# Performance work log

Hardware: AMD Instinct MI355X
Metric: run time of the kernel (lower is better)

## Reference

```python
import jax, jax.numpy as jnp
import numpy as np

STRIDES = (8, 16, 32)
INPUT = (640, 640)
NC = 80           # num_classes
CONF = 0.65       # conf_thr
IOU_THR = 0.65    # nms iou_threshold
K = 1000          # fixed candidate cap for jit-compatible NMS (padded/masked)


def _priors():
    # MlvlPointGenerator(offset=0, with_stride=True): per level, points at
    # (x*stride, y*stride) flattened y-major, format [cx, cy, stride, stride].
    ps = []
    for s in STRIDES:
        H, W = INPUT[0] // s, INPUT[1] // s
        yy, xx = jnp.meshgrid(jnp.arange(H, dtype=jnp.float32),
                              jnp.arange(W, dtype=jnp.float32), indexing='ij')
        cx = (xx * s).ravel()
        cy = (yy * s).ravel()
        st = jnp.full_like(cx, float(s))
        ps.append(jnp.stack([cx, cy, st, st], axis=-1))
    return jnp.concatenate(ps, axis=0)  # [8400, 4]


def _flatten(xs, c):
    # permute(0,2,3,1).reshape(B, -1, c) per level, concat over priors
    return jnp.concatenate(
        [x.transpose(0, 2, 3, 1).reshape(x.shape[0], -1, c) for x in xs], axis=1)


def _decode(priors, bp):
    # bp: [B, N, 4]; priors: [N, 4] (cx, cy, sw, sh)
    xys = bp[..., :2] * priors[:, 2:] + priors[:, :2]
    whs = jnp.exp(bp[..., 2:]) * priors[:, 2:]
    tl = xys - whs * 0.5
    br = xys + whs * 0.5
    return jnp.concatenate([tl, br], axis=-1)  # [B, N, 4] tlbr


def _iou(a, b):
    tl = jnp.maximum(a[:, None, :2], b[None, :, :2])
    br = jnp.minimum(a[:, None, 2:], b[None, :, 2:])
    wh = jnp.clip(br - tl, 0.0)
    inter = wh[..., 0] * wh[..., 1]
    area = lambda x: (x[:, 2] - x[:, 0]) * (x[:, 3] - x[:, 1])
    union = area(a)[:, None] + area(b)[None, :] - inter
    return inter / (union + 1e-6)


def _nms_single(cls_s, obj_s, boxes):
    # cls_s: [N, NC] sigmoid scores; obj_s: [N]; boxes: [N, 4]
    max_s = cls_s.max(axis=-1)
    labels = jnp.argmax(cls_s, axis=-1)
    score = max_s * obj_s
    valid = score >= CONF                       # confidence mask
    sc = jnp.where(valid, score, 0.0)
    top_sc, idx = jax.lax.top_k(sc, K)          # sorted descending -> greedy order
    b = boxes[idx]
    lab = labels[idx]
    v = valid[idx]
    # class-aware (batched) NMS: offset boxes per label so classes never overlap
    max_coord = jnp.max(jnp.abs(b)) + 1.0
    ob = b + (lab.astype(b.dtype) * max_coord)[:, None]
    iou = _iou(ob, ob)                          # [K, K]
    j = jnp.arange(K)
    def body(i, keep):
        sup = (iou[i] > IOU_THR) & (j > i)
        return jnp.where(keep[i] & v[i], keep & (~sup), keep)
    keep = jax.lax.fori_loop(0, K, body, jnp.ones(K, dtype=bool))
    final = keep & v
    dets = jnp.where(final[:, None],
                     jnp.concatenate([b, top_sc[:, None]], axis=-1), 0.0)  # [K, 5]
    labs = jnp.where(final, lab, -1)
    return dets, labs, final


def setup_inputs() -> dict:
    key = jax.random.key(0)
    ks = jax.random.split(key, 9)
    B = 32
    shapes = {
        'cls0': (B, NC, 80, 80), 'cls1': (B, NC, 40, 40), 'cls2': (B, NC, 20, 20),
        'bbox0': (B, 4, 80, 80), 'bbox1': (B, 4, 40, 40), 'bbox2': (B, 4, 20, 20),
        'obj0': (B, 1, 80, 80), 'obj1': (B, 1, 40, 40), 'obj2': (B, 1, 20, 20),
    }
    return {n: jax.random.normal(k, s, dtype=jnp.float32)
            for (n, s), k in zip(shapes.items(), ks)}


def reference(cls0, cls1, cls2, bbox0, bbox1, bbox2, obj0, obj1, obj2):
    priors = _priors()
    cls = jax.nn.sigmoid(_flatten([cls0, cls1, cls2], NC))       # [B, 8400, 80]
    bp = _flatten([bbox0, bbox1, bbox2], 4)                      # [B, 8400, 4]
    obj = jax.nn.sigmoid(_flatten([obj0, obj1, obj2], 1)[..., 0])  # [B, 8400]
    boxes = _decode(priors, bp)                                  # [B, 8400, 4]
    # per-image class-wise batched NMS, padded to K detections
    dets, labels, keep = jax.vmap(_nms_single)(cls, obj, boxes)
    return dets, labels, keep
```

## Files before the change

### kernel.cpp

```cpp
#include <hip/hip_runtime.h>
#include <stdint.h>

#define NPRIOR 8400
#define NB 32
#define NCLS 80
#define KTOP 1000
#define CAP 8400
#define CPAD 16
#define PCH 8
#define CPC 10

typedef unsigned long long u64;

__device__ __forceinline__ float exp_np(float x) {
#pragma clang fp contract(off)
    if (x > 88.72283935546875f) return __builtin_huge_valf();
    if (x < -87.3365478515625f) return 0.0f;
    float q = rintf(x * 1.442695040f);
    float r = fmaf(q, -6.93145752e-1f, x);
    r = fmaf(q, -1.42860677e-6f, r);
    float p = fmaf(1.9875691500e-4f, r, 1.3981999507e-3f);
    p = fmaf(p, r, 8.3334519073e-3f);
    p = fmaf(p, r, 4.1665795894e-2f);
    p = fmaf(p, r, 1.6666665459e-1f);
    p = fmaf(p, r, 5.0000001201e-1f);
    float r2 = r * r;
    p = fmaf(p, r2, r);
    p = p + 1.0f;
    return ldexpf(p, (int)q);
}
__device__ __forceinline__ float sigm_np(float x) {
#pragma clang fp contract(off)
    float t = exp_np(-x);
    return 1.0f / (1.0f + t);
}

__device__ __forceinline__ void level_of(int n, int& W, int& s, int& loc) {
    if (n < 6400)      { W = 80; s = 8;  loc = n; }
    else if (n < 8000) { W = 40; s = 16; loc = n - 6400; }
    else               { W = 20; s = 32; loc = n - 8000; }
}

__device__ float4 decode32(int b, int n,
                           const float* bb0, const float* bb1, const float* bb2) {
#pragma clang fp contract(off)
    int W, s, loc; level_of(n, W, s, loc);
    const float* bb = (s == 8) ? bb0 : (s == 16) ? bb1 : bb2;
    int hw = W * W;
    int y = loc / W, x = loc - y * W;
    const float* bp = bb + (size_t)b * 4 * hw + y * W + x;
    float fs = (float)s;
    float cx = (float)x * fs, cy = (float)y * fs;
    float xc = bp[0] * fs + cx;
    float yc = bp[hw] * fs + cy;
    float wv = exp_np(bp[2 * hw]) * fs;
    float hv = exp_np(bp[3 * hw]) * fs;
    float wv2 = wv * 0.5f, hv2 = hv * 0.5f;
    float4 r;
    r.x = xc - wv2;
    r.y = yc - hv2;
    r.z = xc + wv2;
    r.w = yc + hv2;
    return r;
}

__device__ __forceinline__ u64 packkc(float s, int c) {
    return ((u64)__float_as_uint(s) << 32) | (unsigned)(~(unsigned)c);
}

__global__ void __launch_bounds__(256) score1_k(
    const float* __restrict__ cls0, const float* __restrict__ cls1, const float* __restrict__ cls2,
    u64* __restrict__ part)
{
#pragma clang fp contract(off)
    int b = blockIdx.z, ch = blockIdx.y;
    int g = blockIdx.x * 256 + threadIdx.x;
    if (g >= NPRIOR / 4) return;
    int n0 = g * 4;
    int W, s, loc; level_of(n0, W, s, loc);
    const float* cls = (s == 8) ? cls0 : (s == 16) ? cls1 : cls2;
    int hw = W * W;
    int y = loc / W, x = loc - y * W;
    const float* cp = cls + (size_t)b * NCLS * hw + y * W + x;

    int c0 = ch * CPC;
    float4 v = *(const float4*)(cp + (size_t)c0 * hw);
    u64 k0 = packkc(sigm_np(v.x), c0);
    u64 k1 = packkc(sigm_np(v.y), c0);
    u64 k2 = packkc(sigm_np(v.z), c0);
    u64 k3 = packkc(sigm_np(v.w), c0);
#pragma unroll
    for (int cc = 1; cc < CPC; ++cc) {
        int c = c0 + cc;
        v = *(const float4*)(cp + (size_t)c * hw);
        u64 t;
        t = packkc(sigm_np(v.x), c); if (t > k0) k0 = t;
        t = packkc(sigm_np(v.y), c); if (t > k1) k1 = t;
        t = packkc(sigm_np(v.z), c); if (t > k2) k2 = t;
        t = packkc(sigm_np(v.w), c); if (t > k3) k3 = t;
    }
    u64* p = part + ((size_t)ch * NB + b) * NPRIOR + n0;
    p[0] = k0; p[1] = k1; p[2] = k2; p[3] = k3;
}

__global__ void __launch_bounds__(256) score2_k(
    const float* __restrict__ ob0, const float* __restrict__ ob1, const float* __restrict__ ob2,
    const u64* __restrict__ part,
    float* __restrict__ sc, int* __restrict__ labels,
    u64* __restrict__ keys, int* __restrict__ cnts)
{
#pragma clang fp contract(off)
    int b = blockIdx.y;
    int g = blockIdx.x * 256 + threadIdx.x;
    if (g >= NPRIOR / 4) return;
    int n0 = g * 4;
    int W, s, loc; level_of(n0, W, s, loc);
    const float* ob = (s == 8) ? ob0 : (s == 16) ? ob1 : ob2;
    int hw = W * W;
    int y = loc / W, x = loc - y * W;

    u64 k0 = 0, k1 = 0, k2 = 0, k3 = 0;
#pragma unroll
    for (int ch = 0; ch < PCH; ++ch) {
        const u64* p = part + ((size_t)ch * NB + b) * NPRIOR + n0;
        u64 t0 = p[0], t1 = p[1], t2 = p[2], t3 = p[3];
        if (t0 > k0) k0 = t0;
        if (t1 > k1) k1 = t1;
        if (t2 > k2) k2 = t2;
        if (t3 > k3) k3 = t3;
    }
    float4 tM;
    tM.x = __uint_as_float((unsigned)(k0 >> 32));
    tM.y = __uint_as_float((unsigned)(k1 >> 32));
    tM.z = __uint_as_float((unsigned)(k2 >> 32));
    tM.w = __uint_as_float((unsigned)(k3 >> 32));
    int4 lab;
    lab.x = (int)(~(unsigned)(k0 & 0xffffffffull));
    lab.y = (int)(~(unsigned)(k1 & 0xffffffffull));
    lab.z = (int)(~(unsigned)(k2 & 0xffffffffull));
    lab.w = (int)(~(unsigned)(k3 & 0xffffffffull));

    float4 o = *(const float4*)(ob + (size_t)b * hw + y * W + x);
    float4 sv;
    sv.x = tM.x * sigm_np(o.x);
    sv.y = tM.y * sigm_np(o.y);
    sv.z = tM.z * sigm_np(o.z);
    sv.w = tM.w * sigm_np(o.w);
    float4 scv;
    scv.x = (sv.x >= 0.65f) ? sv.x : 0.0f;
    scv.y = (sv.y >= 0.65f) ? sv.y : 0.0f;
    scv.z = (sv.z >= 0.65f) ? sv.z : 0.0f;
    scv.w = (sv.w >= 0.65f) ? sv.w : 0.0f;
    *(float4*)(sc + (size_t)b * NPRIOR + n0) = scv;
    *(int4*)(labels + (size_t)b * NPRIOR + n0) = lab;

    int lane = threadIdx.x & 63;
#pragma unroll
    for (int e = 0; e < 4; ++e) {
        float se = (e == 0) ? scv.x : (e == 1) ? scv.y : (e == 2) ? scv.z : scv.w;
        bool val = se > 0.0f;
        u64 mb = __ballot(val);
        if (mb) {
            int lead = (int)__builtin_ctzll(mb);
            int base = 0;
            if (lane == lead) base = atomicAdd(&cnts[b * CPAD], (int)__popcll(mb));
            base = __shfl(base, lead);
            if (val) {
                int myoff = (int)__popcll(mb & ((1ull << lane) - 1ull));
                keys[(size_t)b * CAP + base + myoff] =
                    ((u64)__float_as_uint(se) << 32) | (unsigned)(~(unsigned)(n0 + e));
            }
        }
    }
}

__global__ void __launch_bounds__(256) rank_part(
    const u64* __restrict__ keys, const int* __restrict__ cnts,
    int* __restrict__ rankbuf)
{
    int b = blockIdx.y, tid = threadIdx.x;
    int cn = min(cnts[b * CPAD], CAP);
    int nt = (cn + 255) >> 8;
    int ntt = nt * nt;
    const u64* keyimg = keys + (size_t)b * CAP;
    int lane = tid & 63;

    for (int t = blockIdx.x; t < ntt; t += gridDim.x) {
        int it = t / nt, jt = t - it * nt;
        int i = it * 256 + tid;
        u64 ki = (i < cn) ? keyimg[i] : ~0ull;
        int rank = 0;
        int jbase = jt * 256;
        int jend = min(jbase + 256, cn);
        for (int jb = jbase; jb < jend; jb += 64) {
            int j = jb + lane;
            u64 kv = (j < cn) ? keyimg[j] : 0ull;
            unsigned lo = (unsigned)kv, hi = (unsigned)(kv >> 32);
            int lim = jend - jb;
#pragma unroll
            for (int l = 0; l < 64; ++l) {
                unsigned jlo = __builtin_amdgcn_readlane(lo, l);
                unsigned jhi = __builtin_amdgcn_readlane(hi, l);
                u64 kj = ((u64)jhi << 32) | jlo;
                rank += (l < lim && kj > ki) ? 1 : 0;
            }
        }
        if (i < cn && rank > 0) atomicAdd(&rankbuf[(size_t)b * CAP + i], rank);
    }
}

__global__ void __launch_bounds__(256) scatter_k(
    const u64* __restrict__ keys, const int* __restrict__ cnts,
    const int* __restrict__ rankbuf,
    const float* __restrict__ sc, const int* __restrict__ labels,
    const float* __restrict__ bb0, const float* __restrict__ bb1, const float* __restrict__ bb2,
    float4* __restrict__ sel_box, float* __restrict__ sel_score,
    int* __restrict__ sel_label, int* __restrict__ maxbits, u64* __restrict__ vmask)
{
#pragma clang fp contract(off)
    __shared__ float redbuf[256];
    int b = blockIdx.y, chunk = blockIdx.x, tid = threadIdx.x;
    int cn = min(cnts[b * CPAD], CAP);
    int base = chunk * 256;
    if (chunk != 0 && base >= cn) return;

    const u64* keyimg = keys + (size_t)b * CAP;
    const int* labb = labels + (size_t)b * NPRIOR;
    const float* scb = sc + (size_t)b * NPRIOR;

    int i = base + tid;
    float lmax = 0.0f;
    if (i < cn) {
        int rank = rankbuf[(size_t)b * CAP + i];
        if (rank < KTOP) {
            u64 ki = keyimg[i];
            unsigned n = ~(unsigned)(ki & 0xffffffffull);
            float s = __uint_as_float((unsigned)(ki >> 32));
            float4 bx = decode32(b, (int)n, bb0, bb1, bb2);
            sel_box[(size_t)b * 1024 + rank] = bx;
            sel_score[(size_t)b * 1024 + rank] = s;
            sel_label[(size_t)b * 1024 + rank] = labb[n];
            lmax = fmaxf(fmaxf(fabsf(bx.x), fabsf(bx.y)),
                         fmaxf(fabsf(bx.z), fabsf(bx.w)));
        }
    }

    if (chunk == 0) {
        if (cn < KTOP && tid == 0) {
            float lm = 0.0f;
            int r = cn;
            for (int n = 0; n < NPRIOR && r < KTOP; ++n) {
                if (scb[n] == 0.0f) {
                    float4 bx = decode32(b, n, bb0, bb1, bb2);
                    sel_box[(size_t)b * 1024 + r] = bx;
                    sel_score[(size_t)b * 1024 + r] = 0.0f;
                    sel_label[(size_t)b * 1024 + r] = labb[n];
                    lm = fmaxf(lm, fmaxf(fmaxf(fabsf(bx.x), fabsf(bx.y)),
                                         fmaxf(fabsf(bx.z), fabsf(bx.w))));
                    ++r;
                }
            }
            lmax = fmaxf(lmax, lm);
        }
        if (tid < 24) {
            sel_box[(size_t)b * 1024 + 1000 + tid] = make_float4(0.f, 0.f, 0.f, 0.f);
            sel_score[(size_t)b * 1024 + 1000 + tid] = 0.0f;
            sel_label[(size_t)b * 1024 + 1000 + tid] = 0;
        }
        if (tid < 16) {
            int vc = min(cn, KTOP);
            int lo = tid * 64;
            u64 m;
            if (vc >= lo + 64)      m = ~0ull;
            else if (vc <= lo)      m = 0ull;
            else                    m = (1ull << (vc - lo)) - 1ull;
            vmask[b * 16 + tid] = m;
        }
    }

    redbuf[tid] = lmax;
    __syncthreads();
    for (int off = 128; off > 0; off >>= 1) {
        if (tid < off) redbuf[tid] = fmaxf(redbuf[tid], redbuf[tid + off]);
        __syncthreads();
    }
    if (tid == 0) atomicMax(&maxbits[b * CPAD], __float_as_int(redbuf[0]));
}

__global__ void __launch_bounds__(256) build_mask_T(
    const float4* __restrict__ sel_box, const int* __restrict__ sel_label,
    const int* __restrict__ maxbits, u64* __restrict__ Cmask)
{
#pragma clang fp contract(off)
    __shared__ float4 obr[256];
    __shared__ float arr[256];
    int b = blockIdx.y;
    int cg = blockIdx.x & 15, rgq = blockIdx.x >> 4;
    if (rgq * 4 > cg) return;
    int tid = threadIdx.x, wave = tid >> 6, lane = tid & 63;
    float mc = __int_as_float(maxbits[b * CPAD]) + 1.0f;

    {
        int row = rgq * 256 + tid;
        float4 v = sel_box[(size_t)b * 1024 + row];
        float off = (float)sel_label[(size_t)b * 1024 + row] * mc;
        v.x += off; v.y += off; v.z += off; v.w += off;
        obr[tid] = v;
        arr[tid] = (v.z - v.x) * (v.w - v.y);
    }
    int col = cg * 64 + lane;
    float4 a = sel_box[(size_t)b * 1024 + col];
    float offc = (float)sel_label[(size_t)b * 1024 + col] * mc;
    a.x += offc; a.y += offc; a.z += offc; a.w += offc;
    float ac = (a.z - a.x) * (a.w - a.y);
    __syncthreads();

    int rg = rgq * 4 + wave;
    if (rg > cg) return;
    int rowbase = rg * 64;
    u64 bits = 0;
#pragma unroll 8
    for (int r = 0; r < 64; ++r) {
        int row = rowbase + r;
        float4 rb = obr[wave * 64 + r];
        float ra = arr[wave * 64 + r];
        bool pred = false;
        if (row < col && row < KTOP && col < KTOP) {
            float tlx = fmaxf(rb.x, a.x), tly = fmaxf(rb.y, a.y);
            float brx = fminf(rb.z, a.z), bry = fminf(rb.w, a.w);
            float w = fmaxf(brx - tlx, 0.0f), h = fmaxf(bry - tly, 0.0f);
            float inter = w * h;
            float uni = (ra + ac) - inter;
            float iou = inter / (uni + 1e-6f);
            pred = iou > 0.65f;
        }
        bits |= pred ? (1ull << r) : 0ull;
    }
    Cmask[((size_t)b * 16 + rg) * 1024 + col] = bits;
}

__global__ void __launch_bounds__(64) nms_fixpoint_write(
    const u64* __restrict__ Cmask, const u64* __restrict__ vmask,
    const float4* __restrict__ sel_box, const float* __restrict__ sel_score,
    const int* __restrict__ sel_label, float* __restrict__ out)
{
    int b = blockIdx.x, lane = threadIdx.x;
    const u64* Cimg = Cmask + (size_t)b * 16 * 1024;
    u64 Khist[16];
#pragma unroll
    for (int g = 0; g < 16; ++g) {
        int col = g * 64 + lane;
        bool supp = false;
#pragma unroll
        for (int gp = 0; gp < g; ++gp)
            supp |= (Cimg[(size_t)gp * 1024 + col] & Khist[gp]) != 0ull;
        u64 V = vmask[b * 16 + g] & ~__ballot(supp);
        u64 T = Cimg[(size_t)g * 1024 + col];
        u64 K = V;
        for (int it = 0; it < 64; ++it) {
            u64 Knew = V & ~__ballot((T & K) != 0ull);
            if (Knew == K) break;
            K = Knew;
        }
        Khist[g] = K;
    }

    const size_t selo = (size_t)b * 1024;
    float* lab_o = out + (size_t)NB * KTOP * 5;
    float* keep_o = lab_o + (size_t)NB * KTOP;
#pragma unroll
    for (int g = 0; g < 16; ++g) {
        int k = g * 64 + lane;
        if (k >= KTOP) break;
        bool fin = (Khist[g] >> lane) & 1ull;
        float4 bx = sel_box[selo + k];
        float s = sel_score[selo + k];
        int lb = sel_label[selo + k];
        size_t o5 = ((size_t)b * KTOP + k) * 5;
        out[o5 + 0] = fin ? bx.x : 0.0f;
        out[o5 + 1] = fin ? bx.y : 0.0f;
        out[o5 + 2] = fin ? bx.z : 0.0f;
        out[o5 + 3] = fin ? bx.w : 0.0f;
        out[o5 + 4] = fin ? s : 0.0f;
        lab_o[b * KTOP + k] = fin ? (float)lb : -1.0f;
        keep_o[b * KTOP + k] = fin ? 1.0f : 0.0f;
    }
}

extern "C" void kernel_launch(void* const* d_in, const int* in_sizes, int n_in,
                              void* d_out, int out_size, void* d_ws, size_t ws_size,
                              hipStream_t stream) {
    const float* cls0 = (const float*)d_in[0];
    const float* cls1 = (const float*)d_in[1];
    const float* cls2 = (const float*)d_in[2];
    const float* bb0  = (const float*)d_in[3];
    const float* bb1  = (const float*)d_in[4];
    const float* bb2  = (const float*)d_in[5];
    const float* ob0  = (const float*)d_in[6];
    const float* ob1  = (const float*)d_in[7];
    const float* ob2  = (const float*)d_in[8];
    float* out = (float*)d_out;

    char* w = (char*)d_ws;
    size_t used = 0;
    auto alloc = [&](size_t bytes) -> void* {
        void* p = (void*)(w + used);
        used += (bytes + 255) & ~(size_t)255;
        return p;
    };
    float* sc        = (float*)alloc((size_t)NB * NPRIOR * 4);
    int* labels      = (int*)alloc((size_t)NB * NPRIOR * 4);
    u64* keys        = (u64*)alloc((size_t)NB * CAP * 8);
    u64* part        = (u64*)alloc((size_t)PCH * NB * NPRIOR * 8);
    int* zeroed      = (int*)alloc((size_t)(2 * NB * CPAD + NB * CAP) * 4);
    float4* sel_box  = (float4*)alloc((size_t)NB * 1024 * 16);
    float* sel_score = (float*)alloc((size_t)NB * 1024 * 4);
    int* sel_label   = (int*)alloc((size_t)NB * 1024 * 4);
    u64* vmask       = (u64*)alloc((size_t)NB * 16 * 8);
    u64* Cmask       = (u64*)alloc((size_t)NB * 16 * 1024 * 8);

    if (used > ws_size) return;

    int* cnts = zeroed;
    int* maxbits = zeroed + NB * CPAD;
    int* rankbuf = zeroed + 2 * NB * CPAD;
    hipMemsetAsync(zeroed, 0, (size_t)(2 * NB * CPAD + NB * CAP) * 4, stream);

    score1_k<<<dim3((NPRIOR / 4 + 255) / 256, PCH, NB), 256, 0, stream>>>(
        cls0, cls1, cls2, part);
    score2_k<<<dim3((NPRIOR / 4 + 255) / 256, NB), 256, 0, stream>>>(
        ob0, ob1, ob2, part, sc, labels, keys, cnts);
    rank_part<<<dim3(64, NB), 256, 0, stream>>>(keys, cnts, rankbuf);
    scatter_k<<<dim3((CAP + 255) / 256, NB), 256, 0, stream>>>(
        keys, cnts, rankbuf, sc, labels, bb0, bb1, bb2,
        sel_box, sel_score, sel_label, maxbits, vmask);
    build_mask_T<<<dim3(64, NB), 256, 0, stream>>>(sel_box, sel_label, maxbits, Cmask);
    nms_fixpoint_write<<<NB, 64, 0, stream>>>(
        Cmask, vmask, sel_box, sel_score, sel_label, out);
}
```

Measured before the change: 111.3 us.

## Argmax on raw logits with top-2 gap check, drop memset

score1 now finds the per-chunk max on raw logits and tracks the runner-up, so it no longer computes a sigmoid for each of the 80 classes. score2 merges the chunks, applies sigmoid only to the winner, and falls back to a full 80-class sigmoid argmax when the top-2 gap is too small to rule out rounding ties. The memset of counters and rankbuf is replaced by zeroing inside the kernels (counters in score1, rankbuf only at compacted positions in score2). This adds a part2 buffer to write and read and a rare slow fallback path. Zeroing on the fly assumes the counters are cleared before score2's atomics, which holds only because the kernels run in stream order.

```diff
diff --git a/kernel.cpp b/kernel.cpp
--- a/kernel.cpp
+++ b/kernel.cpp
@@ -64,16 +64,27 @@
     return r;
 }
 
-__device__ __forceinline__ u64 packkc(float s, int c) {
-    return ((u64)__float_as_uint(s) << 32) | (unsigned)(~(unsigned)c);
+__device__ __forceinline__ unsigned flt2ord(float f) {
+    unsigned u = __float_as_uint(f);
+    return u ^ ((u >> 31) ? 0xffffffffu : 0x80000000u);
+}
+__device__ __forceinline__ float ord2flt(unsigned u) {
+    u ^= ((u >> 31) ? 0x80000000u : 0xffffffffu);
+    return __uint_as_float(u);
+}
+__device__ __forceinline__ u64 packlc(float l, int c) {
+    return ((u64)flt2ord(l) << 32) | (unsigned)(~(unsigned)c);
 }
 
 __global__ void __launch_bounds__(256) score1_k(
     const float* __restrict__ cls0, const float* __restrict__ cls1, const float* __restrict__ cls2,
-    u64* __restrict__ part)
-{
-#pragma clang fp contract(off)
+    u64* __restrict__ part, float* __restrict__ part2, int* __restrict__ zeroed)
+{
     int b = blockIdx.z, ch = blockIdx.y;
+    if (blockIdx.x == 0 && ch == 0 && threadIdx.x == 0) {
+        zeroed[b * CPAD] = 0;
+        zeroed[NB * CPAD + b * CPAD] = 0;
+    }
     int g = blockIdx.x * 256 + threadIdx.x;
     if (g >= NPRIOR / 4) return;
     int n0 = g * 4;
@@ -85,29 +96,32 @@
 
     int c0 = ch * CPC;
     float4 v = *(const float4*)(cp + (size_t)c0 * hw);
-    u64 k0 = packkc(sigm_np(v.x), c0);
-    u64 k1 = packkc(sigm_np(v.y), c0);
-    u64 k2 = packkc(sigm_np(v.z), c0);
-    u64 k3 = packkc(sigm_np(v.w), c0);
+    float M[4]  = {v.x, v.y, v.z, v.w};
+    float S2[4] = {-3.4e38f, -3.4e38f, -3.4e38f, -3.4e38f};
+    int   I[4]  = {c0, c0, c0, c0};
 #pragma unroll
     for (int cc = 1; cc < CPC; ++cc) {
         int c = c0 + cc;
         v = *(const float4*)(cp + (size_t)c * hw);
-        u64 t;
-        t = packkc(sigm_np(v.x), c); if (t > k0) k0 = t;
-        t = packkc(sigm_np(v.y), c); if (t > k1) k1 = t;
-        t = packkc(sigm_np(v.z), c); if (t > k2) k2 = t;
-        t = packkc(sigm_np(v.w), c); if (t > k3) k3 = t;
+        float l[4] = {v.x, v.y, v.z, v.w};
+#pragma unroll
+        for (int e = 0; e < 4; ++e) {
+            if (l[e] > M[e]) { S2[e] = M[e]; M[e] = l[e]; I[e] = c; }
+            else             { S2[e] = fmaxf(S2[e], l[e]); }
+        }
     }
     u64* p = part + ((size_t)ch * NB + b) * NPRIOR + n0;
-    p[0] = k0; p[1] = k1; p[2] = k2; p[3] = k3;
+    float* p2 = part2 + ((size_t)ch * NB + b) * NPRIOR + n0;
+#pragma unroll
+    for (int e = 0; e < 4; ++e) { p[e] = packlc(M[e], I[e]); p2[e] = S2[e]; }
 }
 
 __global__ void __launch_bounds__(256) score2_k(
+    const float* __restrict__ cls0, const float* __restrict__ cls1, const float* __restrict__ cls2,
     const float* __restrict__ ob0, const float* __restrict__ ob1, const float* __restrict__ ob2,
-    const u64* __restrict__ part,
+    const u64* __restrict__ part, const float* __restrict__ part2,
     float* __restrict__ sc, int* __restrict__ labels,
-    u64* __restrict__ keys, int* __restrict__ cnts)
+    u64* __restrict__ keys, int* __restrict__ cnts, int* __restrict__ rankbuf)
 {
 #pragma clang fp contract(off)
     int b = blockIdx.y;
@@ -115,49 +129,76 @@
     if (g >= NPRIOR / 4) return;
     int n0 = g * 4;
     int W, s, loc; level_of(n0, W, s, loc);
-    const float* ob = (s == 8) ? ob0 : (s == 16) ? ob1 : ob2;
+    const float* cls = (s == 8) ? cls0 : (s == 16) ? cls1 : cls2;
+    const float* ob  = (s == 8) ? ob0  : (s == 16) ? ob1  : ob2;
     int hw = W * W;
     int y = loc / W, x = loc - y * W;
 
-    u64 k0 = 0, k1 = 0, k2 = 0, k3 = 0;
+    u64 P[PCH][4];
+    float Z[PCH][4];
 #pragma unroll
     for (int ch = 0; ch < PCH; ++ch) {
         const u64* p = part + ((size_t)ch * NB + b) * NPRIOR + n0;
-        u64 t0 = p[0], t1 = p[1], t2 = p[2], t3 = p[3];
-        if (t0 > k0) k0 = t0;
-        if (t1 > k1) k1 = t1;
-        if (t2 > k2) k2 = t2;
-        if (t3 > k3) k3 = t3;
-    }
-    float4 tM;
-    tM.x = __uint_as_float((unsigned)(k0 >> 32));
-    tM.y = __uint_as_float((unsigned)(k1 >> 32));
-    tM.z = __uint_as_float((unsigned)(k2 >> 32));
-    tM.w = __uint_as_float((unsigned)(k3 >> 32));
-    int4 lab;
-    lab.x = (int)(~(unsigned)(k0 & 0xffffffffull));
-    lab.y = (int)(~(unsigned)(k1 & 0xffffffffull));
-    lab.z = (int)(~(unsigned)(k2 & 0xffffffffull));
-    lab.w = (int)(~(unsigned)(k3 & 0xffffffffull));
+        const float* p2 = part2 + ((size_t)ch * NB + b) * NPRIOR + n0;
+#pragma unroll
+        for (int e = 0; e < 4; ++e) { P[ch][e] = p[e]; Z[ch][e] = p2[e]; }
+    }
+    u64 best[4];
+#pragma unroll
+    for (int e = 0; e < 4; ++e) {
+        u64 bp = P[0][e];
+#pragma unroll
+        for (int ch = 1; ch < PCH; ++ch) bp = (P[ch][e] > bp) ? P[ch][e] : bp;
+        best[e] = bp;
+    }
+    float m2g[4];
+#pragma unroll
+    for (int e = 0; e < 4; ++e) {
+        float m2 = -3.4e38f;
+#pragma unroll
+        for (int ch = 0; ch < PCH; ++ch) {
+            bool win = (P[ch][e] == best[e]);
+            float cand = win ? Z[ch][e] : ord2flt((unsigned)(P[ch][e] >> 32));
+            m2 = fmaxf(m2, cand);
+        }
+        m2g[e] = m2;
+    }
+
+    float tMv[4]; int labv[4];
+#pragma unroll
+    for (int e = 0; e < 4; ++e) {
+        float M = ord2flt((unsigned)(best[e] >> 32));
+        int lab = (int)(~(unsigned)(best[e] & 0xffffffffull));
+        float tM = sigm_np(M);
+        float gap = M - m2g[e];
+        float mx = fmaxf(fabsf(M), fabsf(m2g[e]));
+        bool safe = (gap * exp_np(-mx)) > 1.6e-5f;
+        if (!safe) {
+            const float* cpe = cls + (size_t)b * NCLS * hw + y * W + x + e;
+            tM = sigm_np(cpe[0]); lab = 0;
+            for (int c = 1; c < NCLS; ++c) {
+                float t = sigm_np(cpe[(size_t)c * hw]);
+                if (t > tM) { tM = t; lab = c; }
+            }
+        }
+        tMv[e] = tM; labv[e] = lab;
+    }
 
     float4 o = *(const float4*)(ob + (size_t)b * hw + y * W + x);
-    float4 sv;
-    sv.x = tM.x * sigm_np(o.x);
-    sv.y = tM.y * sigm_np(o.y);
-    sv.z = tM.z * sigm_np(o.z);
-    sv.w = tM.w * sigm_np(o.w);
-    float4 scv;
-    scv.x = (sv.x >= 0.65f) ? sv.x : 0.0f;
-    scv.y = (sv.y >= 0.65f) ? sv.y : 0.0f;
-    scv.z = (sv.z >= 0.65f) ? sv.z : 0.0f;
-    scv.w = (sv.w >= 0.65f) ? sv.w : 0.0f;
-    *(float4*)(sc + (size_t)b * NPRIOR + n0) = scv;
-    *(int4*)(labels + (size_t)b * NPRIOR + n0) = lab;
+    float so[4] = {sigm_np(o.x), sigm_np(o.y), sigm_np(o.z), sigm_np(o.w)};
+    float scv[4];
+#pragma unroll
+    for (int e = 0; e < 4; ++e) {
+        float sv = tMv[e] * so[e];
+        scv[e] = (sv >= 0.65f) ? sv : 0.0f;
+    }
+    *(float4*)(sc + (size_t)b * NPRIOR + n0) = make_float4(scv[0], scv[1], scv[2], scv[3]);
+    *(int4*)(labels + (size_t)b * NPRIOR + n0) = make_int4(labv[0], labv[1], labv[2], labv[3]);
 
     int lane = threadIdx.x & 63;
 #pragma unroll
     for (int e = 0; e < 4; ++e) {
-        float se = (e == 0) ? scv.x : (e == 1) ? scv.y : (e == 2) ? scv.z : scv.w;
+        float se = scv[e];
         bool val = se > 0.0f;
         u64 mb = __ballot(val);
         if (mb) {
@@ -167,8 +208,10 @@
             base = __shfl(base, lead);
             if (val) {
                 int myoff = (int)__popcll(mb & ((1ull << lane) - 1ull));
-                keys[(size_t)b * CAP + base + myoff] =
+                int pos = base + myoff;
+                keys[(size_t)b * CAP + pos] =
                     ((u64)__float_as_uint(se) << 32) | (unsigned)(~(unsigned)(n0 + e));
+                rankbuf[(size_t)b * CAP + pos] = 0;
             }
         }
     }
@@ -412,7 +455,9 @@
     int* labels      = (int*)alloc((size_t)NB * NPRIOR * 4);
     u64* keys        = (u64*)alloc((size_t)NB * CAP * 8);
     u64* part        = (u64*)alloc((size_t)PCH * NB * NPRIOR * 8);
-    int* zeroed      = (int*)alloc((size_t)(2 * NB * CPAD + NB * CAP) * 4);
+    float* part2     = (float*)alloc((size_t)PCH * NB * NPRIOR * 4);
+    int* zeroed      = (int*)alloc((size_t)2 * NB * CPAD * 4);
+    int* rankbuf     = (int*)alloc((size_t)NB * CAP * 4);
     float4* sel_box  = (float4*)alloc((size_t)NB * 1024 * 16);
     float* sel_score = (float*)alloc((size_t)NB * 1024 * 4);
     int* sel_label   = (int*)alloc((size_t)NB * 1024 * 4);
@@ -423,13 +468,12 @@
 
     int* cnts = zeroed;
     int* maxbits = zeroed + NB * CPAD;
-    int* rankbuf = zeroed + 2 * NB * CPAD;
-    hipMemsetAsync(zeroed, 0, (size_t)(2 * NB * CPAD + NB * CAP) * 4, stream);
 
     score1_k<<<dim3((NPRIOR / 4 + 255) / 256, PCH, NB), 256, 0, stream>>>(
-        cls0, cls1, cls2, part);
+        cls0, cls1, cls2, part, part2, zeroed);
     score2_k<<<dim3((NPRIOR / 4 + 255) / 256, NB), 256, 0, stream>>>(
-        ob0, ob1, ob2, part, sc, labels, keys, cnts);
+        cls0, cls1, cls2, ob0, ob1, ob2, part, part2,
+        sc, labels, keys, cnts, rankbuf);
     rank_part<<<dim3(64, NB), 256, 0, stream>>>(keys, cnts, rankbuf);
     scatter_k<<<dim3((CAP + 255) / 256, NB), 256, 0, stream>>>(
         keys, cnts, rankbuf, sc, labels, bb0, bb1, bb2,
```

Result: slower. 154.9 us (+39.2%).

## Fuse class-max and objectness scoring into one kernel with logit-space argmax

Applied to the files above, without the earlier changes.

Merges the two scoring kernels into one that scans all 80 class logits per prior, tracks the max and second-max in logit space, and applies the sigmoid only once. When the top two logits are too close for the sigmoid ordering to be trusted, it falls back to an exact per-class sigmoid scan. This removes the partial-max buffer round trip through global memory. The large memset is replaced by a tiny init kernel plus zeroing only the rankbuf slots that are actually used. Trade-offs: each thread now handles one prior with scalar strided loads instead of float4, and the tie-break fallback adds a divergent path.

```diff
diff --git a/kernel.cpp b/kernel.cpp
--- a/kernel.cpp
+++ b/kernel.cpp
@@ -7,8 +7,6 @@
 #define KTOP 1000
 #define CAP 8400
 #define CPAD 16
-#define PCH 8
-#define CPC 10
 
 typedef unsigned long long u64;
 
@@ -64,112 +62,74 @@
     return r;
 }
 
-__device__ __forceinline__ u64 packkc(float s, int c) {
-    return ((u64)__float_as_uint(s) << 32) | (unsigned)(~(unsigned)c);
-}
-
-__global__ void __launch_bounds__(256) score1_k(
+__global__ void __launch_bounds__(64) init_k(int* __restrict__ cnts_mb) {
+    cnts_mb[threadIdx.x * CPAD] = 0;
+}
+
+__global__ void __launch_bounds__(256) score_k(
     const float* __restrict__ cls0, const float* __restrict__ cls1, const float* __restrict__ cls2,
-    u64* __restrict__ part)
-{
-#pragma clang fp contract(off)
-    int b = blockIdx.z, ch = blockIdx.y;
-    int g = blockIdx.x * 256 + threadIdx.x;
-    if (g >= NPRIOR / 4) return;
-    int n0 = g * 4;
-    int W, s, loc; level_of(n0, W, s, loc);
+    const float* __restrict__ ob0,  const float* __restrict__ ob1,  const float* __restrict__ ob2,
+    float* __restrict__ sc, int* __restrict__ labels,
+    u64* __restrict__ keys, int* __restrict__ cnts, int* __restrict__ rankbuf)
+{
+#pragma clang fp contract(off)
+    int b = blockIdx.y;
+    int n = blockIdx.x * 256 + threadIdx.x;
+    bool nvalid = (n < NPRIOR);
+    int nc = nvalid ? n : NPRIOR - 1;
+    int W, s, loc; level_of(nc, W, s, loc);
     const float* cls = (s == 8) ? cls0 : (s == 16) ? cls1 : cls2;
+    const float* ob  = (s == 8) ? ob0  : (s == 16) ? ob1  : ob2;
     int hw = W * W;
     int y = loc / W, x = loc - y * W;
     const float* cp = cls + (size_t)b * NCLS * hw + y * W + x;
 
-    int c0 = ch * CPC;
-    float4 v = *(const float4*)(cp + (size_t)c0 * hw);
-    u64 k0 = packkc(sigm_np(v.x), c0);
-    u64 k1 = packkc(sigm_np(v.y), c0);
-    u64 k2 = packkc(sigm_np(v.z), c0);
-    u64 k3 = packkc(sigm_np(v.w), c0);
-#pragma unroll
-    for (int cc = 1; cc < CPC; ++cc) {
-        int c = c0 + cc;
-        v = *(const float4*)(cp + (size_t)c * hw);
-        u64 t;
-        t = packkc(sigm_np(v.x), c); if (t > k0) k0 = t;
-        t = packkc(sigm_np(v.y), c); if (t > k1) k1 = t;
-        t = packkc(sigm_np(v.z), c); if (t > k2) k2 = t;
-        t = packkc(sigm_np(v.w), c); if (t > k3) k3 = t;
-    }
-    u64* p = part + ((size_t)ch * NB + b) * NPRIOR + n0;
-    p[0] = k0; p[1] = k1; p[2] = k2; p[3] = k3;
-}
-
-__global__ void __launch_bounds__(256) score2_k(
-    const float* __restrict__ ob0, const float* __restrict__ ob1, const float* __restrict__ ob2,
-    const u64* __restrict__ part,
-    float* __restrict__ sc, int* __restrict__ labels,
-    u64* __restrict__ keys, int* __restrict__ cnts)
-{
-#pragma clang fp contract(off)
-    int b = blockIdx.y;
-    int g = blockIdx.x * 256 + threadIdx.x;
-    if (g >= NPRIOR / 4) return;
-    int n0 = g * 4;
-    int W, s, loc; level_of(n0, W, s, loc);
-    const float* ob = (s == 8) ? ob0 : (s == 16) ? ob1 : ob2;
-    int hw = W * W;
-    int y = loc / W, x = loc - y * W;
-
-    u64 k0 = 0, k1 = 0, k2 = 0, k3 = 0;
-#pragma unroll
-    for (int ch = 0; ch < PCH; ++ch) {
-        const u64* p = part + ((size_t)ch * NB + b) * NPRIOR + n0;
-        u64 t0 = p[0], t1 = p[1], t2 = p[2], t3 = p[3];
-        if (t0 > k0) k0 = t0;
-        if (t1 > k1) k1 = t1;
-        if (t2 > k2) k2 = t2;
-        if (t3 > k3) k3 = t3;
-    }
-    float4 tM;
-    tM.x = __uint_as_float((unsigned)(k0 >> 32));
-    tM.y = __uint_as_float((unsigned)(k1 >> 32));
-    tM.z = __uint_as_float((unsigned)(k2 >> 32));
-    tM.w = __uint_as_float((unsigned)(k3 >> 32));
-    int4 lab;
-    lab.x = (int)(~(unsigned)(k0 & 0xffffffffull));
-    lab.y = (int)(~(unsigned)(k1 & 0xffffffffull));
-    lab.z = (int)(~(unsigned)(k2 & 0xffffffffull));
-    lab.w = (int)(~(unsigned)(k3 & 0xffffffffull));
-
-    float4 o = *(const float4*)(ob + (size_t)b * hw + y * W + x);
-    float4 sv;
-    sv.x = tM.x * sigm_np(o.x);
-    sv.y = tM.y * sigm_np(o.y);
-    sv.z = tM.z * sigm_np(o.z);
-    sv.w = tM.w * sigm_np(o.w);
-    float4 scv;
-    scv.x = (sv.x >= 0.65f) ? sv.x : 0.0f;
-    scv.y = (sv.y >= 0.65f) ? sv.y : 0.0f;
-    scv.z = (sv.z >= 0.65f) ? sv.z : 0.0f;
-    scv.w = (sv.w >= 0.65f) ? sv.w : 0.0f;
-    *(float4*)(sc + (size_t)b * NPRIOR + n0) = scv;
-    *(int4*)(labels + (size_t)b * NPRIOR + n0) = lab;
+    float M = -3.4e38f, S2 = -3.4e38f;
+    int I = 0;
+    for (int cb = 0; cb < NCLS; cb += 8) {
+        float buf[8];
+#pragma unroll
+        for (int k = 0; k < 8; ++k) buf[k] = cp[(size_t)(cb + k) * hw];
+#pragma unroll
+        for (int k = 0; k < 8; ++k) {
+            float l = buf[k];
+            if (l > M) { S2 = M; M = l; I = cb + k; }
+            else       { S2 = fmaxf(S2, l); }
+        }
+    }
+
+    float tM = sigm_np(M);
+    int lab = I;
+    float gap = M - S2;
+    float mx = fmaxf(fabsf(M), fabsf(S2));
+    if (!((gap * exp_np(-mx)) > 1.6e-5f)) {
+        tM = -1.0f; lab = 0;
+        for (int c = 0; c < NCLS; ++c) {
+            float t = sigm_np(cp[(size_t)c * hw]);
+            if (t > tM) { tM = t; lab = c; }
+        }
+    }
+    float sObj = sigm_np(ob[(size_t)b * hw + y * W + x]);
+    float score = tM * sObj;
+    float scv = (score >= 0.65f) ? score : 0.0f;
+    if (nvalid) {
+        sc[(size_t)b * NPRIOR + n] = scv;
+        labels[(size_t)b * NPRIOR + n] = lab;
+    }
 
     int lane = threadIdx.x & 63;
-#pragma unroll
-    for (int e = 0; e < 4; ++e) {
-        float se = (e == 0) ? scv.x : (e == 1) ? scv.y : (e == 2) ? scv.z : scv.w;
-        bool val = se > 0.0f;
-        u64 mb = __ballot(val);
-        if (mb) {
-            int lead = (int)__builtin_ctzll(mb);
-            int base = 0;
-            if (lane == lead) base = atomicAdd(&cnts[b * CPAD], (int)__popcll(mb));
-            base = __shfl(base, lead);
-            if (val) {
-                int myoff = (int)__popcll(mb & ((1ull << lane) - 1ull));
-                keys[(size_t)b * CAP + base + myoff] =
-                    ((u64)__float_as_uint(se) << 32) | (unsigned)(~(unsigned)(n0 + e));
-            }
+    bool val = nvalid && (scv > 0.0f);
+    u64 mb = __ballot(val);
+    if (mb) {
+        int lead = (int)__builtin_ctzll(mb);
+        int base = 0;
+        if (lane == lead) base = atomicAdd(&cnts[b * CPAD], (int)__popcll(mb));
+        base = __shfl(base, lead);
+        if (val) {
+            int pos = base + (int)__popcll(mb & ((1ull << lane) - 1ull));
+            keys[(size_t)b * CAP + pos] =
+                ((u64)__float_as_uint(scv) << 32) | (unsigned)(~(unsigned)n);
+            rankbuf[(size_t)b * CAP + pos] = 0;
         }
     }
 }
@@ -317,8 +277,8 @@
 
     int rg = rgq * 4 + wave;
     if (rg > cg) return;
+    u64 bits = 0;
     int rowbase = rg * 64;
-    u64 bits = 0;
 #pragma unroll 8
     for (int r = 0; r < 64; ++r) {
         int row = rowbase + r;
@@ -411,8 +371,8 @@
     float* sc        = (float*)alloc((size_t)NB * NPRIOR * 4);
     int* labels      = (int*)alloc((size_t)NB * NPRIOR * 4);
     u64* keys        = (u64*)alloc((size_t)NB * CAP * 8);
-    u64* part        = (u64*)alloc((size_t)PCH * NB * NPRIOR * 8);
-    int* zeroed      = (int*)alloc((size_t)(2 * NB * CPAD + NB * CAP) * 4);
+    int* cnts_mb     = (int*)alloc((size_t)2 * NB * CPAD * 4);
+    int* rankbuf     = (int*)alloc((size_t)NB * CAP * 4);
     float4* sel_box  = (float4*)alloc((size_t)NB * 1024 * 16);
     float* sel_score = (float*)alloc((size_t)NB * 1024 * 4);
     int* sel_label   = (int*)alloc((size_t)NB * 1024 * 4);
@@ -421,15 +381,12 @@
 
     if (used > ws_size) return;
 
-    int* cnts = zeroed;
-    int* maxbits = zeroed + NB * CPAD;
-    int* rankbuf = zeroed + 2 * NB * CPAD;
-    hipMemsetAsync(zeroed, 0, (size_t)(2 * NB * CPAD + NB * CAP) * 4, stream);
-
-    score1_k<<<dim3((NPRIOR / 4 + 255) / 256, PCH, NB), 256, 0, stream>>>(
-        cls0, cls1, cls2, part);
-    score2_k<<<dim3((NPRIOR / 4 + 255) / 256, NB), 256, 0, stream>>>(
-        ob0, ob1, ob2, part, sc, labels, keys, cnts);
+    int* cnts = cnts_mb;
+    int* maxbits = cnts_mb + NB * CPAD;
+
+    init_k<<<1, 64, 0, stream>>>(cnts_mb);
+    score_k<<<dim3((NPRIOR + 255) / 256, NB), 256, 0, stream>>>(
+        cls0, cls1, cls2, ob0, ob1, ob2, sc, labels, keys, cnts, rankbuf);
     rank_part<<<dim3(64, NB), 256, 0, stream>>>(keys, cnts, rankbuf);
     scatter_k<<<dim3((CAP + 255) / 256, NB), 256, 0, stream>>>(
         keys, cnts, rankbuf, sc, labels, bb0, bb1, bb2,
```

New measurement: 117.8 us. 5.8% more time.
